# Performance work log

Hardware: AMD Instinct MI355X
Metric: run time of the kernel (lower is better)

The kernel has to match this reference:

```python
import jax, jax.numpy as jnp
import numpy as np

NUM_CLASSES = 80
TOP_K = 9
BG_IDX = NUM_CLASSES
NUM_ANCHORS_LIST = [6400, 1600, 400]  # strides 8/16/32 on 640x640 input
BS = 32
N_MAX = 64
EPS = 1e-9


def _make_anchors():
    boxes = []
    for stride, n_side in [(8, 80), (16, 40), (32, 20)]:
        xs = (np.arange(n_side, dtype=np.float32) + 0.5) * stride
        cy, cx = np.meshgrid(xs, xs, indexing='ij')
        cx = cx.reshape(-1); cy = cy.reshape(-1)
        half = stride * 2.5
        boxes.append(np.stack([cx - half, cy - half, cx + half, cy + half], axis=-1))
    return jnp.asarray(np.concatenate(boxes, 0), dtype=jnp.float32)  # [8400,4]


def setup_inputs() -> dict:
    key = jax.random.key(0)
    k1, k2, k3, k4 = jax.random.split(key, 4)
    anchors = _make_anchors()
    lt = jax.random.uniform(k1, (BS, N_MAX, 2), minval=0.0, maxval=500.0)
    wh = jax.random.uniform(k2, (BS, N_MAX, 2), minval=8.0, maxval=140.0)
    gt_boxes = jnp.concatenate([lt, lt + wh], axis=-1)  # valid x1<x2,y1<y2
    labels = jax.random.randint(k3, (BS, N_MAX), 0, NUM_CLASSES)
    mask_gt = jnp.ones((BS, N_MAX, 1), jnp.float32)
    pred = anchors[None, :, :] + 10.0 * jax.random.normal(k4, (BS, anchors.shape[0], 4))
    return dict(anchors_xx_yy=anchors, num_anchors_list=NUM_ANCHORS_LIST,
                ground_true_labels=labels, ground_true_xx_yy=gt_boxes,
                mask_ground_true=mask_gt, predict_xy_xy=pred)


def _pairwise_iou(b1, b2):
    # b1 [...,M,4], b2 [...,N,4] -> [...,M,N]
    lt = jnp.maximum(b1[..., :, None, :2], b2[..., None, :, :2])
    rb = jnp.minimum(b1[..., :, None, 2:], b2[..., None, :, 2:])
    wh = jnp.clip(rb - lt, 0.0)
    inter = wh[..., 0] * wh[..., 1]
    a1 = (b1[..., 2] - b1[..., 0]) * (b1[..., 3] - b1[..., 1])
    a2 = (b2[..., 2] - b2[..., 0]) * (b2[..., 3] - b2[..., 1])
    return inter / (a1[..., :, None] + a2[..., None, :] - inter + 1e-9)


def reference(anchors_xx_yy, num_anchors_list, ground_true_labels, ground_true_xx_yy,
              mask_ground_true, predict_xy_xy):
    num_anchors_list = [int(n) for n in np.asarray(num_anchors_list)]
    bs, n_max, _ = ground_true_xx_yy.shape
    n_anchors = anchors_xx_yy.shape[0]
    gt_flat = ground_true_xx_yy.reshape(-1, 4)

    # pairwise IoU gt x anchors, and center L2 distances
    overlaps = _pairwise_iou(gt_flat, anchors_xx_yy).reshape(bs, n_max, n_anchors)
    ac_points = 0.5 * (anchors_xx_yy[:, :2] + anchors_xx_yy[:, 2:])      # [A,2]
    gt_centers = 0.5 * (gt_flat[:, :2] + gt_flat[:, 2:])                 # [bs*nmax,2]
    distances = jnp.linalg.norm(gt_centers[:, None, :] - ac_points[None, :, :], axis=-1)
    distances = distances.reshape(bs, n_max, n_anchors)

    # per-level top-k closest candidates
    mask_gt_bool = mask_ground_true > 0  # [bs,nmax,1]
    is_in_list, idx_list, start = [], [], 0
    for na in num_anchors_list:
        k = min(TOP_K, na)
        d = distances[..., start:start + na]
        _, idx = jax.lax.top_k(-d, k)                       # smallest distances
        idx_list.append(idx + start)
        idx_m = jnp.where(mask_gt_bool, idx, 0)
        cnt = jax.nn.one_hot(idx_m, na, dtype=distances.dtype).sum(axis=-2)
        is_in_list.append(jnp.where(cnt > 1, 0.0, cnt))
        start += na
    is_in_candidate = jnp.concatenate(is_in_list, axis=-1)   # [bs,nmax,A]
    candidate_idx = jnp.concatenate(idx_list, axis=-1)       # [bs,nmax,L*k]

    # ATSS threshold: mean + std (unbiased, as torch) of candidate IoUs
    iou_candidates = jnp.where(is_in_candidate > 0, overlaps, 0.0)
    gathered = jnp.take_along_axis(iou_candidates, candidate_idx, axis=-1)
    thr = gathered.mean(axis=-1, keepdims=True) + gathered.std(axis=-1, keepdims=True, ddof=1)
    is_pos = jnp.where(iou_candidates > thr, is_in_candidate, 0.0)

    # anchor centers inside gt boxes
    d_lt = (ac_points[None, None, :, :] - ground_true_xx_yy[:, :, None, :2]).min(axis=-1)
    d_rb = (ground_true_xx_yy[:, :, None, 2:] - ac_points[None, None, :, :]).min(axis=-1)
    is_in_gts = (jnp.minimum(d_lt, d_rb) > EPS).astype(overlaps.dtype)

    mask_pos = is_pos * is_in_gts * mask_ground_true

    # resolve anchors assigned to multiple gts by max overlap
    fg = mask_pos.sum(axis=-2)                               # [bs,A]
    multi = fg[:, None, :] > 1
    is_max = jax.nn.one_hot(overlaps.argmax(axis=1), n_max, dtype=overlaps.dtype)
    is_max = jnp.transpose(is_max, (0, 2, 1))                # [bs,nmax,A]
    mask_pos = jnp.where(multi, is_max, mask_pos)
    fg_mask = mask_pos.sum(axis=-2)
    target_gt_idx = mask_pos.argmax(axis=-2)                 # [bs,A]

    # gather targets
    flat_idx = (target_gt_idx + jnp.arange(bs)[:, None] * n_max).reshape(-1)
    t_labels = ground_true_labels.reshape(-1)[flat_idx].reshape(bs, n_anchors)
    t_labels = jnp.where(fg_mask > 0, t_labels, BG_IDX)
    t_boxes = gt_flat[flat_idx].reshape(bs, n_anchors, 4)
    t_scores = jax.nn.one_hot(t_labels, NUM_CLASSES + 1, dtype=jnp.float32)[..., :NUM_CLASSES]

    # scale scores by max predicted IoU per anchor among positive gts
    pred_iou = _pairwise_iou(ground_true_xx_yy, predict_xy_xy) * mask_pos
    iou_max = pred_iou.max(axis=-2)[..., None]               # [bs,A,1]
    t_scores = t_scores * iou_max

    return (t_labels.astype(jnp.int32), t_boxes, t_scores, fg_mask > 0)
```

## Files before the change

kernel.cpp:

```cpp
#include <hip/hip_runtime.h>
#include <float.h>

#define NA_TOTAL 8400
#define BSZ 32
#define NMAX 64
#define BG_IDX 80

__device__ __forceinline__ float iou_pair(float ax1, float ay1, float ax2, float ay2,
                                          float bx1, float by1, float bx2, float by2) {
#pragma clang fp contract(off)
  float ltx = fmaxf(ax1, bx1);
  float lty = fmaxf(ay1, by1);
  float rbx = fminf(ax2, bx2);
  float rby = fminf(ay2, by2);
  float w = fmaxf(rbx - ltx, 0.0f);
  float h = fmaxf(rby - lty, 0.0f);
  float inter = w * h;
  float a1 = (ax2 - ax1) * (ay2 - ay1);
  float a2 = (bx2 - bx1) * (by2 - by1);
  return inter / (a1 + a2 - inter + 1e-9f);
}

__global__ __launch_bounds__(256) void stage1_kernel(
    const float* __restrict__ anchors,
    const float* __restrict__ gt_boxes,
    const float* __restrict__ mask_gt,
    int* __restrict__ pos_list) {
#pragma clang fp contract(off)
  const int lane = threadIdx.x & 63;
  const int wid = threadIdx.x >> 6;
  const int t = blockIdx.x * 4 + wid;

  if (mask_gt[t] <= 0.0f) {
    if (lane < 27) pos_list[t * 27 + lane] = -1;
    return;
  }

  const float4 gtb = ((const float4*)gt_boxes)[t];
  const float gx1 = gtb.x, gy1 = gtb.y, gx2 = gtb.z, gy2 = gtb.w;
  const float gcx = 0.5f * (gx1 + gx2);
  const float gcy = 0.5f * (gy1 + gy2);

  float io_arr[3];
  int aidx[3];
  bool sel_arr[3];
  unsigned long long bal[3];

#pragma unroll
  for (int lv = 0; lv < 3; ++lv) {
    const int strd = (lv == 0) ? 8 : (lv == 1) ? 16 : 32;
    const int n = (lv == 0) ? 80 : (lv == 1) ? 40 : 20;
    const int startA = (lv == 0) ? 0 : (lv == 1) ? 6400 : 8000;
    const float inv = 1.0f / (float)strd;

    int ix0 = (int)floorf(gcx * inv);
    int iy0 = (int)floorf(gcy * inv);
    ix0 = min(max(ix0, 0), n - 1);
    iy0 = min(max(iy0, 0), n - 1);
    int wx0 = min(max(ix0 - 2, 0), n - 5);
    int wy0 = min(max(iy0 - 2, 0), n - 5);

    int a = startA + (wy0 + lane / 5) * n + (wx0 + lane % 5);
    aidx[lv] = a;
    float d = FLT_MAX;
    float iov = 0.0f;
    if (lane < 25) {
      float4 ab = ((const float4*)anchors)[a];
      float acx = 0.5f * (ab.x + ab.z);
      float acy = 0.5f * (ab.y + ab.w);
      float dx = gcx - acx;
      float dy = gcy - acy;
      d = sqrtf(dx * dx + dy * dy);
      iov = iou_pair(gx1, gy1, gx2, gy2, ab.x, ab.y, ab.z, ab.w);
    }
    io_arr[lv] = iov;

    int cnt = 0;
    for (int j = 0; j < 25; ++j) {
      float dj = __shfl(d, j);
      cnt += (int)((dj < d) | ((dj == d) & (j < lane)));
    }
    bool sel = (lane < 25) && (cnt < 9);
    sel_arr[lv] = sel;
    bal[lv] = __ballot(sel);
  }

  double s = 0.0;
#pragma unroll
  for (int lv = 0; lv < 3; ++lv) {
    for (int j = 0; j < 25; ++j) {
      float v = __shfl(io_arr[lv], j);
      s += ((bal[lv] >> j) & 1ull) ? (double)v : 0.0;
    }
  }
  double mean = s / 27.0;
  double s2 = 0.0;
#pragma unroll
  for (int lv = 0; lv < 3; ++lv) {
    for (int j = 0; j < 25; ++j) {
      float v = __shfl(io_arr[lv], j);
      double dd = (double)v - mean;
      s2 += ((bal[lv] >> j) & 1ull) ? dd * dd : 0.0;
    }
  }
  float thr = (float)(mean + sqrt(s2 / 26.0));

#pragma unroll
  for (int lv = 0; lv < 3; ++lv) {
    if (sel_arr[lv]) {
      int rank = (int)__popcll(bal[lv] & ((1ull << lane) - 1ull));
      int val = -1;
      if (io_arr[lv] > thr) {
        int a = aidx[lv];
        float4 ab = ((const float4*)anchors)[a];
        float acx = 0.5f * (ab.x + ab.z);
        float acy = 0.5f * (ab.y + ab.w);
        float d_in = fminf(fminf(acx - gx1, acy - gy1), fminf(gx2 - acx, gy2 - acy));
        if (d_in > 1e-9f) val = a;
      }
      pos_list[t * 27 + lv * 9 + rank] = val;
    }
  }
}

__global__ __launch_bounds__(256) void stage2_kernel(
    const float* __restrict__ anchors,
    const float* __restrict__ gt_boxes,
    const int* __restrict__ labels,
    const float* __restrict__ pred,
    const int* __restrict__ pos_list,
    float* __restrict__ out_lab,
    float* __restrict__ out_box,
    float4* __restrict__ out_sco4,
    float* __restrict__ out_fgm) {
#pragma clang fp contract(off)
  const int b = blockIdx.y;
  const int A0 = blockIdx.x * 256;
  const int tid = threadIdx.x;
  const int a = A0 + tid;

  __shared__ float4 gts[64];
  __shared__ int labs[64];
  __shared__ unsigned mLo[256];
  __shared__ unsigned mHi[256];
  __shared__ int plist[64 * 27];
  __shared__ int lab_s[256];
  __shared__ float im_s[256];

  if (tid < 64) {
    gts[tid] = ((const float4*)gt_boxes)[b * 64 + tid];
    labs[tid] = labels[b * 64 + tid];
  }
  mLo[tid] = 0u;
  mHi[tid] = 0u;
  for (int i = tid; i < 64 * 27; i += 256) plist[i] = pos_list[b * 64 * 27 + i];
  __syncthreads();

  for (int i = tid; i < 64 * 27; i += 256) {
    int av = plist[i];
    if (av >= A0 && av < A0 + 256) {
      int g = i / 27;
      int la = av - A0;
      if (g < 32) atomicOr(&mLo[la], 1u << g);
      else        atomicOr(&mHi[la], 1u << (g - 32));
    }
  }
  __syncthreads();

  const bool valid = a < NA_TOTAL;
  int lab = BG_IDX;
  float im = 0.0f;
  if (valid) {
    unsigned long long bits =
        (unsigned long long)mLo[tid] | ((unsigned long long)mHi[tid] << 32);
    int fg = __popcll(bits);
    bool pos = fg > 0;
    int target = 0;
    if (fg == 1) {
      target = __builtin_ctzll(bits);
    } else if (fg > 1) {
      float4 ab = ((const float4*)anchors)[a];
      float best = -1.0f;
      int bi = 0;
      for (int g2 = 0; g2 < 64; ++g2) {
        float4 gb = gts[g2];
        float v = iou_pair(gb.x, gb.y, gb.z, gb.w, ab.x, ab.y, ab.z, ab.w);
        if (v > best) { best = v; bi = g2; }
      }
      target = bi;
    }
    lab = pos ? labs[target] : BG_IDX;
    const size_t idx = (size_t)b * NA_TOTAL + a;
    out_lab[idx] = (float)lab;
    float4 tb = gts[target];
    ((float4*)out_box)[idx] = tb;
    out_fgm[idx] = pos ? 1.0f : 0.0f;
    if (pos) {
      float4 pb = ((const float4*)pred)[idx];
      im = iou_pair(tb.x, tb.y, tb.z, tb.w, pb.x, pb.y, pb.z, pb.w);
    }
  }
  lab_s[tid] = lab;
  im_s[tid] = im;
  __syncthreads();

  const int ntile = min(NA_TOTAL - A0, 256);
  const int nval = ntile * 20;
  const size_t base = (size_t)b * NA_TOTAL * 20 + (size_t)A0 * 20;
  for (int k = tid; k < nval; k += 256) {
    int la = k / 20;
    int q = k - la * 20;
    int lb = lab_s[la];
    float v_im = im_s[la];
    int c0 = q * 4;
    float4 v;
    v.x = (lb == c0 + 0) ? v_im : 0.0f;
    v.y = (lb == c0 + 1) ? v_im : 0.0f;
    v.z = (lb == c0 + 2) ? v_im : 0.0f;
    v.w = (lb == c0 + 3) ? v_im : 0.0f;
    out_sco4[base + k] = v;
  }
}

extern "C" void kernel_launch(void* const* d_in, const int* in_sizes, int n_in,
                              void* d_out, int out_size, void* d_ws, size_t ws_size,
                              hipStream_t stream) {
  const float* anchors = (const float*)d_in[0];
  const int* labels = (const int*)d_in[2];
  const float* gt_boxes = (const float*)d_in[3];
  const float* mask_gt = (const float*)d_in[4];
  const float* pred = (const float*)d_in[5];

  float* out = (float*)d_out;
  float* out_lab = out;
  float* out_box = out + (size_t)BSZ * NA_TOTAL;
  float* out_sco = out + (size_t)BSZ * NA_TOTAL * 5;
  float* out_fgm = out + (size_t)BSZ * NA_TOTAL * 85;

  int* pos_list = (int*)d_ws;

  stage1_kernel<<<(BSZ * NMAX) / 4, 256, 0, stream>>>(anchors, gt_boxes, mask_gt,
                                                      pos_list);

  dim3 g2((NA_TOTAL + 255) / 256, BSZ);
  stage2_kernel<<<g2, 256, 0, stream>>>(anchors, gt_boxes, labels, pred, pos_list,
                                        out_lab, out_box, (float4*)out_sco, out_fgm);
}
```

Measured before the change: 33.92 us.

## Use nontemporal stores, wave-shuffle score writes, and hoist pred/anchor loads

Stage 2 now loads the pred and anchor boxes for every thread up front, before the shared-memory setup, so their latency overlaps the pos_list scan. The shared lab/im arrays and the block barrier before the score write are dropped. Each wavefront instead writes its own 64 anchors' 80-class score rows, fetching label and IoU through lane shuffles, in a fully unrolled loop. All output writes use nontemporal stores to avoid polluting the cache with the large write-only output, at the cost of loading pred even for anchors that end up as background.

```diff
diff --git a/kernel.cpp b/kernel.cpp
--- a/kernel.cpp
+++ b/kernel.cpp
@@ -5,6 +5,15 @@
 #define BSZ 32
 #define NMAX 64
 #define BG_IDX 80
+
+typedef float f32x4 __attribute__((ext_vector_type(4)));
+
+__device__ __forceinline__ void nt_store4(float x, float y, float z, float w,
+                                          float* p) {
+  f32x4 v;
+  v.x = x; v.y = y; v.z = z; v.w = w;
+  __builtin_nontemporal_store(v, (f32x4*)p);
+}
 
 __device__ __forceinline__ float iou_pair(float ax1, float ay1, float ax2, float ay2,
                                           float bx1, float by1, float bx2, float by2) {
@@ -131,21 +140,26 @@
     const int* __restrict__ pos_list,
     float* __restrict__ out_lab,
     float* __restrict__ out_box,
-    float4* __restrict__ out_sco4,
+    float* __restrict__ out_sco,
     float* __restrict__ out_fgm) {
 #pragma clang fp contract(off)
   const int b = blockIdx.y;
   const int A0 = blockIdx.x * 256;
   const int tid = threadIdx.x;
+  const int lane = tid & 63;
+  const int wv = tid >> 6;
   const int a = A0 + tid;
+  const bool valid = a < NA_TOTAL;
 
   __shared__ float4 gts[64];
   __shared__ int labs[64];
   __shared__ unsigned mLo[256];
   __shared__ unsigned mHi[256];
   __shared__ int plist[64 * 27];
-  __shared__ int lab_s[256];
-  __shared__ float im_s[256];
+
+  const size_t idx = (size_t)b * NA_TOTAL + (valid ? a : 0);
+  const float4 pb = ((const float4*)pred)[idx];
+  const float4 ab = ((const float4*)anchors)[valid ? a : 0];
 
   if (tid < 64) {
     gts[tid] = ((const float4*)gt_boxes)[b * 64 + tid];
@@ -167,19 +181,17 @@
   }
   __syncthreads();
 
-  const bool valid = a < NA_TOTAL;
   int lab = BG_IDX;
   float im = 0.0f;
-  if (valid) {
+  {
     unsigned long long bits =
         (unsigned long long)mLo[tid] | ((unsigned long long)mHi[tid] << 32);
     int fg = __popcll(bits);
-    bool pos = fg > 0;
+    bool pos = valid && (fg > 0);
     int target = 0;
     if (fg == 1) {
       target = __builtin_ctzll(bits);
     } else if (fg > 1) {
-      float4 ab = ((const float4*)anchors)[a];
       float best = -1.0f;
       int bi = 0;
       for (int g2 = 0; g2 < 64; ++g2) {
@@ -189,36 +201,35 @@
       }
       target = bi;
     }
-    lab = pos ? labs[target] : BG_IDX;
-    const size_t idx = (size_t)b * NA_TOTAL + a;
-    out_lab[idx] = (float)lab;
     float4 tb = gts[target];
-    ((float4*)out_box)[idx] = tb;
-    out_fgm[idx] = pos ? 1.0f : 0.0f;
     if (pos) {
-      float4 pb = ((const float4*)pred)[idx];
+      lab = labs[target];
       im = iou_pair(tb.x, tb.y, tb.z, tb.w, pb.x, pb.y, pb.z, pb.w);
     }
-  }
-  lab_s[tid] = lab;
-  im_s[tid] = im;
-  __syncthreads();
-
-  const int ntile = min(NA_TOTAL - A0, 256);
-  const int nval = ntile * 20;
-  const size_t base = (size_t)b * NA_TOTAL * 20 + (size_t)A0 * 20;
-  for (int k = tid; k < nval; k += 256) {
+    if (valid) {
+      __builtin_nontemporal_store((float)lab, &out_lab[idx]);
+      nt_store4(tb.x, tb.y, tb.z, tb.w, &out_box[idx * 4]);
+      __builtin_nontemporal_store(pos ? 1.0f : 0.0f, &out_fgm[idx]);
+    }
+  }
+
+  const int awave0 = A0 + (wv << 6);
+  const size_t sbase = ((size_t)b * NA_TOTAL + (size_t)awave0) * 80;
+#pragma unroll
+  for (int it = 0; it < 20; ++it) {
+    int k = (it << 6) + lane;
     int la = k / 20;
     int q = k - la * 20;
-    int lb = lab_s[la];
-    float v_im = im_s[la];
-    int c0 = q * 4;
-    float4 v;
-    v.x = (lb == c0 + 0) ? v_im : 0.0f;
-    v.y = (lb == c0 + 1) ? v_im : 0.0f;
-    v.z = (lb == c0 + 2) ? v_im : 0.0f;
-    v.w = (lb == c0 + 3) ? v_im : 0.0f;
-    out_sco4[base + k] = v;
+    int lb = __shfl(lab, la);
+    float vim = __shfl(im, la);
+    if (awave0 + la < NA_TOTAL) {
+      int c0 = q * 4;
+      nt_store4((lb == c0 + 0) ? vim : 0.0f,
+                (lb == c0 + 1) ? vim : 0.0f,
+                (lb == c0 + 2) ? vim : 0.0f,
+                (lb == c0 + 3) ? vim : 0.0f,
+                &out_sco[sbase + (size_t)k * 4]);
+    }
   }
 }
 
@@ -244,5 +255,5 @@
 
   dim3 g2((NA_TOTAL + 255) / 256, BSZ);
   stage2_kernel<<<g2, 256, 0, stream>>>(anchors, gt_boxes, labels, pred, pos_list,
-                                        out_lab, out_box, (float4*)out_sco, out_fgm);
-}
+                                        out_lab, out_box, out_sco, out_fgm);
+}
```

After: 35.18 us. +3.7%, slower.

## Fuse candidate selection and assignment into one kernel with larger anchor tiles

Applied to the files above, without the earlier changes.

Merges the per-GT top-k/threshold stage into the per-anchor assignment kernel, so each block recomputes the candidate lists for the GTs whose windows overlap its tile and keeps them in shared memory. This drops the second launch and the workspace round trip. Tiles grow to 1050 anchors with 1024-thread blocks, giving a grid of 8x32 blocks. The cost is redundant stage-1 work across blocks and lower parallelism (256 blocks of 1024 threads), plus serialized GT processing per wave.

```diff
diff --git a/kernel.cpp b/kernel.cpp
--- a/kernel.cpp
+++ b/kernel.cpp
@@ -5,6 +5,8 @@
 #define BSZ 32
 #define NMAX 64
 #define BG_IDX 80
+#define TILE 1050
+#define NBLK 8
 
 __device__ __forceinline__ float iou_pair(float ax1, float ay1, float ax2, float ay2,
                                           float bx1, float by1, float bx2, float by2) {
@@ -21,144 +23,148 @@
   return inter / (a1 + a2 - inter + 1e-9f);
 }
 
-__global__ __launch_bounds__(256) void stage1_kernel(
+__global__ __launch_bounds__(1024) void fused_kernel(
     const float* __restrict__ anchors,
     const float* __restrict__ gt_boxes,
     const float* __restrict__ mask_gt,
-    int* __restrict__ pos_list) {
-#pragma clang fp contract(off)
-  const int lane = threadIdx.x & 63;
-  const int wid = threadIdx.x >> 6;
-  const int t = blockIdx.x * 4 + wid;
-
-  if (mask_gt[t] <= 0.0f) {
-    if (lane < 27) pos_list[t * 27 + lane] = -1;
-    return;
-  }
-
-  const float4 gtb = ((const float4*)gt_boxes)[t];
-  const float gx1 = gtb.x, gy1 = gtb.y, gx2 = gtb.z, gy2 = gtb.w;
-  const float gcx = 0.5f * (gx1 + gx2);
-  const float gcy = 0.5f * (gy1 + gy2);
-
-  float io_arr[3];
-  int aidx[3];
-  bool sel_arr[3];
-  unsigned long long bal[3];
-
-#pragma unroll
-  for (int lv = 0; lv < 3; ++lv) {
-    const int strd = (lv == 0) ? 8 : (lv == 1) ? 16 : 32;
-    const int n = (lv == 0) ? 80 : (lv == 1) ? 40 : 20;
-    const int startA = (lv == 0) ? 0 : (lv == 1) ? 6400 : 8000;
-    const float inv = 1.0f / (float)strd;
-
-    int ix0 = (int)floorf(gcx * inv);
-    int iy0 = (int)floorf(gcy * inv);
-    ix0 = min(max(ix0, 0), n - 1);
-    iy0 = min(max(iy0, 0), n - 1);
-    int wx0 = min(max(ix0 - 2, 0), n - 5);
-    int wy0 = min(max(iy0 - 2, 0), n - 5);
-
-    int a = startA + (wy0 + lane / 5) * n + (wx0 + lane % 5);
-    aidx[lv] = a;
-    float d = FLT_MAX;
-    float iov = 0.0f;
-    if (lane < 25) {
-      float4 ab = ((const float4*)anchors)[a];
-      float acx = 0.5f * (ab.x + ab.z);
-      float acy = 0.5f * (ab.y + ab.w);
-      float dx = gcx - acx;
-      float dy = gcy - acy;
-      d = sqrtf(dx * dx + dy * dy);
-      iov = iou_pair(gx1, gy1, gx2, gy2, ab.x, ab.y, ab.z, ab.w);
-    }
-    io_arr[lv] = iov;
-
-    int cnt = 0;
-    for (int j = 0; j < 25; ++j) {
-      float dj = __shfl(d, j);
-      cnt += (int)((dj < d) | ((dj == d) & (j < lane)));
-    }
-    bool sel = (lane < 25) && (cnt < 9);
-    sel_arr[lv] = sel;
-    bal[lv] = __ballot(sel);
-  }
-
-  double s = 0.0;
-#pragma unroll
-  for (int lv = 0; lv < 3; ++lv) {
-    for (int j = 0; j < 25; ++j) {
-      float v = __shfl(io_arr[lv], j);
-      s += ((bal[lv] >> j) & 1ull) ? (double)v : 0.0;
-    }
-  }
-  double mean = s / 27.0;
-  double s2 = 0.0;
-#pragma unroll
-  for (int lv = 0; lv < 3; ++lv) {
-    for (int j = 0; j < 25; ++j) {
-      float v = __shfl(io_arr[lv], j);
-      double dd = (double)v - mean;
-      s2 += ((bal[lv] >> j) & 1ull) ? dd * dd : 0.0;
-    }
-  }
-  float thr = (float)(mean + sqrt(s2 / 26.0));
-
-#pragma unroll
-  for (int lv = 0; lv < 3; ++lv) {
-    if (sel_arr[lv]) {
-      int rank = (int)__popcll(bal[lv] & ((1ull << lane) - 1ull));
-      int val = -1;
-      if (io_arr[lv] > thr) {
-        int a = aidx[lv];
-        float4 ab = ((const float4*)anchors)[a];
-        float acx = 0.5f * (ab.x + ab.z);
-        float acy = 0.5f * (ab.y + ab.w);
-        float d_in = fminf(fminf(acx - gx1, acy - gy1), fminf(gx2 - acx, gy2 - acy));
-        if (d_in > 1e-9f) val = a;
-      }
-      pos_list[t * 27 + lv * 9 + rank] = val;
-    }
-  }
-}
-
-__global__ __launch_bounds__(256) void stage2_kernel(
-    const float* __restrict__ anchors,
-    const float* __restrict__ gt_boxes,
     const int* __restrict__ labels,
     const float* __restrict__ pred,
-    const int* __restrict__ pos_list,
     float* __restrict__ out_lab,
     float* __restrict__ out_box,
     float4* __restrict__ out_sco4,
     float* __restrict__ out_fgm) {
 #pragma clang fp contract(off)
   const int b = blockIdx.y;
-  const int A0 = blockIdx.x * 256;
+  const int A0 = blockIdx.x * TILE;
   const int tid = threadIdx.x;
-  const int a = A0 + tid;
-
+  const int lane = tid & 63;
+  const int wid = tid >> 6;
+
+  __shared__ int plist[NMAX * 27];
+  __shared__ unsigned mLo[TILE + 6];
+  __shared__ unsigned mHi[TILE + 6];
   __shared__ float4 gts[64];
   __shared__ int labs[64];
-  __shared__ unsigned mLo[256];
-  __shared__ unsigned mHi[256];
-  __shared__ int plist[64 * 27];
-  __shared__ int lab_s[256];
-  __shared__ float im_s[256];
+  __shared__ int lab_s[TILE + 6];
+  __shared__ float im_s[TILE + 6];
 
   if (tid < 64) {
     gts[tid] = ((const float4*)gt_boxes)[b * 64 + tid];
     labs[tid] = labels[b * 64 + tid];
   }
-  mLo[tid] = 0u;
-  mHi[tid] = 0u;
-  for (int i = tid; i < 64 * 27; i += 256) plist[i] = pos_list[b * 64 * 27 + i];
-  __syncthreads();
-
-  for (int i = tid; i < 64 * 27; i += 256) {
+  for (int i = tid; i < NMAX * 27; i += 1024) plist[i] = -1;
+  for (int i = tid; i < TILE; i += 1024) { mLo[i] = 0u; mHi[i] = 0u; }
+  __syncthreads();
+
+  for (int gg = 0; gg < 4; ++gg) {
+    const int g = (wid << 2) | gg;
+    const int t = b * 64 + g;
+    if (mask_gt[t] <= 0.0f) continue;
+
+    const float4 gtb = ((const float4*)gt_boxes)[t];
+    const float gx1 = gtb.x, gy1 = gtb.y, gx2 = gtb.z, gy2 = gtb.w;
+    const float gcx = 0.5f * (gx1 + gx2);
+    const float gcy = 0.5f * (gy1 + gy2);
+
+    int wx0s[3], wy0s[3];
+    bool qual = false;
+#pragma unroll
+    for (int lv = 0; lv < 3; ++lv) {
+      const int strd = (lv == 0) ? 8 : (lv == 1) ? 16 : 32;
+      const int n = (lv == 0) ? 80 : (lv == 1) ? 40 : 20;
+      const int startA = (lv == 0) ? 0 : (lv == 1) ? 6400 : 8000;
+      const float inv = 1.0f / (float)strd;
+      int ix0 = (int)floorf(gcx * inv);
+      int iy0 = (int)floorf(gcy * inv);
+      ix0 = min(max(ix0, 0), n - 1);
+      iy0 = min(max(iy0, 0), n - 1);
+      int wx0 = min(max(ix0 - 2, 0), n - 5);
+      int wy0 = min(max(iy0 - 2, 0), n - 5);
+      wx0s[lv] = wx0;
+      wy0s[lv] = wy0;
+      int lo = startA + wy0 * n + wx0;
+      int hi = startA + (wy0 + 4) * n + wx0 + 4;
+      qual = qual || ((hi >= A0) && (lo < A0 + TILE));
+    }
+    if (!qual) continue;
+
+    float io_arr[3];
+    int aidx[3];
+    bool sel_arr[3];
+    unsigned long long bal[3];
+
+#pragma unroll
+    for (int lv = 0; lv < 3; ++lv) {
+      const int n = (lv == 0) ? 80 : (lv == 1) ? 40 : 20;
+      const int startA = (lv == 0) ? 0 : (lv == 1) ? 6400 : 8000;
+      const int wx0 = wx0s[lv], wy0 = wy0s[lv];
+
+      int a = startA + (wy0 + lane / 5) * n + (wx0 + lane % 5);
+      aidx[lv] = a;
+      float d = FLT_MAX;
+      float iov = 0.0f;
+      if (lane < 25) {
+        float4 ab = ((const float4*)anchors)[a];
+        float acx = 0.5f * (ab.x + ab.z);
+        float acy = 0.5f * (ab.y + ab.w);
+        float dx = gcx - acx;
+        float dy = gcy - acy;
+        d = sqrtf(dx * dx + dy * dy);
+        iov = iou_pair(gx1, gy1, gx2, gy2, ab.x, ab.y, ab.z, ab.w);
+      }
+      io_arr[lv] = iov;
+
+      int cnt = 0;
+      for (int j = 0; j < 25; ++j) {
+        float dj = __shfl(d, j);
+        cnt += (int)((dj < d) | ((dj == d) & (j < lane)));
+      }
+      bool sel = (lane < 25) && (cnt < 9);
+      sel_arr[lv] = sel;
+      bal[lv] = __ballot(sel);
+    }
+
+    double s = 0.0;
+#pragma unroll
+    for (int lv = 0; lv < 3; ++lv)
+      for (int j = 0; j < 25; ++j) {
+        float v = __shfl(io_arr[lv], j);
+        s += ((bal[lv] >> j) & 1ull) ? (double)v : 0.0;
+      }
+    double mean = s / 27.0;
+    double s2 = 0.0;
+#pragma unroll
+    for (int lv = 0; lv < 3; ++lv)
+      for (int j = 0; j < 25; ++j) {
+        float v = __shfl(io_arr[lv], j);
+        double dd = (double)v - mean;
+        s2 += ((bal[lv] >> j) & 1ull) ? dd * dd : 0.0;
+      }
+    float thr = (float)(mean + sqrt(s2 / 26.0));
+
+#pragma unroll
+    for (int lv = 0; lv < 3; ++lv) {
+      if (sel_arr[lv]) {
+        int rank = (int)__popcll(bal[lv] & ((1ull << lane) - 1ull));
+        int val = -1;
+        if (io_arr[lv] > thr) {
+          int a = aidx[lv];
+          float4 ab = ((const float4*)anchors)[a];
+          float acx = 0.5f * (ab.x + ab.z);
+          float acy = 0.5f * (ab.y + ab.w);
+          float d_in = fminf(fminf(acx - gx1, acy - gy1),
+                             fminf(gx2 - acx, gy2 - acy));
+          if (d_in > 1e-9f) val = a;
+        }
+        plist[g * 27 + lv * 9 + rank] = val;
+      }
+    }
+  }
+  __syncthreads();
+
+  for (int i = tid; i < NMAX * 27; i += 1024) {
     int av = plist[i];
-    if (av >= A0 && av < A0 + 256) {
+    if (av >= A0 && av < A0 + TILE) {
       int g = i / 27;
       int la = av - A0;
       if (g < 32) atomicOr(&mLo[la], 1u << g);
@@ -167,47 +173,48 @@
   }
   __syncthreads();
 
-  const bool valid = a < NA_TOTAL;
-  int lab = BG_IDX;
-  float im = 0.0f;
-  if (valid) {
-    unsigned long long bits =
-        (unsigned long long)mLo[tid] | ((unsigned long long)mHi[tid] << 32);
-    int fg = __popcll(bits);
-    bool pos = fg > 0;
-    int target = 0;
-    if (fg == 1) {
-      target = __builtin_ctzll(bits);
-    } else if (fg > 1) {
-      float4 ab = ((const float4*)anchors)[a];
-      float best = -1.0f;
-      int bi = 0;
-      for (int g2 = 0; g2 < 64; ++g2) {
-        float4 gb = gts[g2];
-        float v = iou_pair(gb.x, gb.y, gb.z, gb.w, ab.x, ab.y, ab.z, ab.w);
-        if (v > best) { best = v; bi = g2; }
-      }
-      target = bi;
-    }
-    lab = pos ? labs[target] : BG_IDX;
-    const size_t idx = (size_t)b * NA_TOTAL + a;
-    out_lab[idx] = (float)lab;
-    float4 tb = gts[target];
-    ((float4*)out_box)[idx] = tb;
-    out_fgm[idx] = pos ? 1.0f : 0.0f;
-    if (pos) {
-      float4 pb = ((const float4*)pred)[idx];
-      im = iou_pair(tb.x, tb.y, tb.z, tb.w, pb.x, pb.y, pb.z, pb.w);
-    }
-  }
-  lab_s[tid] = lab;
-  im_s[tid] = im;
-  __syncthreads();
-
-  const int ntile = min(NA_TOTAL - A0, 256);
-  const int nval = ntile * 20;
-  const size_t base = (size_t)b * NA_TOTAL * 20 + (size_t)A0 * 20;
-  for (int k = tid; k < nval; k += 256) {
+  for (int base = 0; base < TILE; base += 1024) {
+    int la = base + tid;
+    if (la < TILE) {
+      int a = A0 + la;
+      const size_t idx = (size_t)b * NA_TOTAL + a;
+      unsigned long long bits =
+          (unsigned long long)mLo[la] | ((unsigned long long)mHi[la] << 32);
+      int fg = __popcll(bits);
+      bool pos = fg > 0;
+      int target = 0;
+      if (fg == 1) {
+        target = __builtin_ctzll(bits);
+      } else if (fg > 1) {
+        float4 ab = ((const float4*)anchors)[a];
+        float best = -1.0f;
+        int bi = 0;
+        for (int g2 = 0; g2 < 64; ++g2) {
+          float4 gb = gts[g2];
+          float v = iou_pair(gb.x, gb.y, gb.z, gb.w, ab.x, ab.y, ab.z, ab.w);
+          if (v > best) { best = v; bi = g2; }
+        }
+        target = bi;
+      }
+      int lab = pos ? labs[target] : BG_IDX;
+      out_lab[idx] = (float)lab;
+      float4 tb = gts[target];
+      ((float4*)out_box)[idx] = tb;
+      out_fgm[idx] = pos ? 1.0f : 0.0f;
+      float im = 0.0f;
+      if (pos) {
+        float4 pb = ((const float4*)pred)[idx];
+        im = iou_pair(tb.x, tb.y, tb.z, tb.w, pb.x, pb.y, pb.z, pb.w);
+      }
+      lab_s[la] = lab;
+      im_s[la] = im;
+    }
+  }
+  __syncthreads();
+
+  const int nval = TILE * 20;
+  const size_t sbase = ((size_t)b * NA_TOTAL + (size_t)A0) * 20;
+  for (int k = tid; k < nval; k += 1024) {
     int la = k / 20;
     int q = k - la * 20;
     int lb = lab_s[la];
@@ -218,7 +225,7 @@
     v.y = (lb == c0 + 1) ? v_im : 0.0f;
     v.z = (lb == c0 + 2) ? v_im : 0.0f;
     v.w = (lb == c0 + 3) ? v_im : 0.0f;
-    out_sco4[base + k] = v;
+    out_sco4[sbase + k] = v;
   }
 }
 
@@ -237,12 +244,8 @@
   float* out_sco = out + (size_t)BSZ * NA_TOTAL * 5;
   float* out_fgm = out + (size_t)BSZ * NA_TOTAL * 85;
 
-  int* pos_list = (int*)d_ws;
-
-  stage1_kernel<<<(BSZ * NMAX) / 4, 256, 0, stream>>>(anchors, gt_boxes, mask_gt,
-                                                      pos_list);
-
-  dim3 g2((NA_TOTAL + 255) / 256, BSZ);
-  stage2_kernel<<<g2, 256, 0, stream>>>(anchors, gt_boxes, labels, pred, pos_list,
-                                        out_lab, out_box, (float4*)out_sco, out_fgm);
+  dim3 grid(NBLK, BSZ);
+  fused_kernel<<<grid, 1024, 0, stream>>>(anchors, gt_boxes, mask_gt, labels,
+                                          pred, out_lab, out_box,
+                                          (float4*)out_sco, out_fgm);
 }
```

Result: slower. 117.6 us (+246.9%).
